# Kernel tuning notes

Hardware: AMD Instinct MI355X
Metric: run time of the kernel (lower is better)

Reference implementation:

```python
import jax, jax.numpy as jnp
import numpy as np

FS = 44100.0
# Time-constant bounds (seconds) hard-coded from RC component values in __init__
T_AF_MIN, T_AF_MAX = 820.0 * 4.7e-07 * 0.8, 270000.0 * 4.7e-07 * 1.2
T_AS_MIN, T_AS_MAX = 820.0 * 6.8e-06 * 0.8, 270000.0 * 6.8e-06 * 100.0
T_SF_MIN, T_SF_MAX = 91000.0 * 4.7e-07 * 0.8, 1200000.0 * 4.7e-07 * 1.2
T_SS_MIN, T_SS_MAX = 750000.0 * 6.8e-06 * 0.8, 750000.0 * 6.8e-06 * 100.0


def _logit(p):
    p = min(max(p, 1e-06), 1.0 - 1e-06)
    return float(np.log(p / (1.0 - p)))


def _u_from_seconds(val_s, tmin, tmax):
    return _logit((val_s - tmin) / (tmax - tmin))


def setup_inputs() -> dict:
    key = jax.random.key(0)
    B, T = 128, 131072
    # dB-domain peak envelope, roughly -60..+10 dB so the -24 dB threshold is exercised
    x = jax.random.normal(key, (B, T), dtype=jnp.float32) * 12.0 - 18.0
    return {
        'x_peak_dB': x,
        'comp_thresh': jnp.float32(-24.0),
        'ratio_logit': jnp.float32(np.log(4.0 - 1.0)),
        'fb_logit': jnp.float32(_logit(0.5)),
        'u_T_af': jnp.float32(_u_from_seconds(0.01, T_AF_MIN, T_AF_MAX)),
        'u_T_as': jnp.float32(_u_from_seconds(0.05, T_AS_MIN, T_AS_MAX)),
        'u_T_sf': jnp.float32(_u_from_seconds(0.03, T_SF_MIN, T_SF_MAX)),
        'u_T_ss': jnp.float32(_u_from_seconds(0.2, T_SS_MIN, T_SS_MAX)),
    }


def _secs(u, tmin, tmax):
    return tmin + (tmax - tmin) * jax.nn.sigmoid(u)


def _ssl_comp_gain(x, comp_thresh, ratio_logit, fb_logit, u_T_af, u_T_as, u_T_sf, u_T_ss):
    # Parameter reparameterization (matches module.forward)
    cr = jnp.maximum(jnp.exp(ratio_logit) + 1.0, 1.0 + 1e-04)
    fb = jnp.clip(jax.nn.sigmoid(fb_logit), 0.0, 1.0)
    a_af = jnp.exp(-1.0 / (FS * _secs(u_T_af, T_AF_MIN, T_AF_MAX)))
    a_as = jnp.exp(-1.0 / (FS * _secs(u_T_as, T_AS_MIN, T_AS_MAX)))
    a_sf = jnp.exp(-1.0 / (FS * _secs(u_T_sf, T_SF_MIN, T_SF_MAX)))
    a_ss = jnp.exp(-1.0 / (FS * _secs(u_T_ss, T_SS_MIN, T_SS_MAX)))
    slope = 1.0 - 1.0 / cr

    B = x.shape[0]
    z = jnp.zeros((B,), x.dtype)

    def step(carry, x_t):
        ef, es, y_prev = carry  # fast/slow envelope states (dB reduction, >=0), prev gain (dB)
        lvl = x_t + fb * y_prev              # feedback sidechain level (dB)
        tgt = jnp.maximum(lvl - comp_thresh, 0.0) * slope  # target gain reduction (dB)
        e = 0.5 * (ef + es)
        att = tgt > e                        # hard gate: attack vs shunt (release)
        af = jnp.where(att, a_af, a_sf)
        as_ = jnp.where(att, a_as, a_ss)
        ef = af * ef + (1.0 - af) * tgt
        es = as_ * es + (1.0 - as_) * tgt
        y = -0.5 * (ef + es)                 # gain in dB (<= 0)
        return (ef, es, y), y

    _, ys = jax.lax.scan(step, (z, z, z), x.T)  # scan over time, x.T: (T, B)
    return ys.T  # (B, T)


def reference(x_peak_dB, comp_thresh, ratio_logit, fb_logit, u_T_af, u_T_as, u_T_sf, u_T_ss):
    return _ssl_comp_gain(x_peak_dB.astype(jnp.float32), comp_thresh, ratio_logit,
                          fb_logit, u_T_af, u_T_as, u_T_sf, u_T_ss)
```

## Files before the change

kernel.cpp:

```cpp
#include <hip/hip_runtime.h>
#include <hip/hip_fp16.h>
#include <math.h>


constexpr int   T_LEN    = 131072;
constexpr int   NCM      = 64;
constexpr int   CM       = T_LEN / NCM;
constexpr int   SUB      = 16;
constexpr int   NC       = NCM * SUB;
constexpr int   CF       = T_LEN / NC;
constexpr int   K        = 16;
constexpr float STEP_ES  = 8.0f / 15.0f;
constexpr float INV_STEP = 15.0f / 8.0f;
constexpr int   DPF      = 8;
constexpr int   NV_ROW   = T_LEN >> 2;
constexpr int   NH_ROW   = T_LEN >> 3;
constexpr int   QROW     = T_LEN >> 2;
constexpr int   LINK     = NCM * K;

__device__ void compute_params(
        float* __restrict__ pw,
        const float* cth, const float* rl, const float* fbl,
        const float* uaf, const float* uas, const float* usf, const float* uss)
{
    const double FS = 44100.0;
    const double T_AF_MIN = 820.0 * 4.7e-07 * 0.8,   T_AF_MAX = 270000.0 * 4.7e-07 * 1.2;
    const double T_AS_MIN = 820.0 * 6.8e-06 * 0.8,   T_AS_MAX = 270000.0 * 6.8e-06 * 100.0;
    const double T_SF_MIN = 91000.0 * 4.7e-07 * 0.8, T_SF_MAX = 1200000.0 * 4.7e-07 * 1.2;
    const double T_SS_MIN = 750000.0 * 6.8e-06 * 0.8, T_SS_MAX = 750000.0 * 6.8e-06 * 100.0;

    double cr    = fmax(exp((double)rl[0]) + 1.0, 1.0 + 1e-4);
    double fb    = 1.0 / (1.0 + exp(-(double)fbl[0]));
    double slope = 1.0 - 1.0 / cr;

    double s_af = T_AF_MIN + (T_AF_MAX - T_AF_MIN) / (1.0 + exp(-(double)uaf[0]));
    double s_as = T_AS_MIN + (T_AS_MAX - T_AS_MIN) / (1.0 + exp(-(double)uas[0]));
    double s_sf = T_SF_MIN + (T_SF_MAX - T_SF_MIN) / (1.0 + exp(-(double)usf[0]));
    double s_ss = T_SS_MIN + (T_SS_MAX - T_SS_MIN) / (1.0 + exp(-(double)uss[0]));

    float a_af = (float)exp(-1.0 / (FS * s_af));
    float a_as = (float)exp(-1.0 / (FS * s_as));
    float a_sf = (float)exp(-1.0 / (FS * s_sf));
    float a_ss = (float)exp(-1.0 / (FS * s_ss));
    double q = 0.5 * slope * fb;

    pw[0]  = (float)(-0.5 * slope);
    pw[1]  = (float)(0.5 * slope * (double)cth[0]);
    pw[2]  = (float)(-q);
    pw[3]  = (float)(0.5 + q);
    pw[4]  = a_af;  pw[5] = a_as;  pw[6] = a_sf;  pw[7] = a_ss;
    float e_af = a_af * a_af, e_as = a_as * a_as, e_sf = a_sf * a_sf, e_ss = a_ss * a_ss;
    pw[8]  = e_af * e_af;  pw[9]  = e_as * e_as;
    pw[10] = e_sf * e_sf;  pw[11] = e_ss * e_ss;
    pw[12] = (float)(-0.125 * slope);
}

__device__ __forceinline__ void aff_compose(float4& A, float2& g,
                                            const float4 Bq, const float2 bg)
{
    float nx = Bq.x * A.x + Bq.y * A.z, ny = Bq.x * A.y + Bq.y * A.w;
    float nz = Bq.z * A.x + Bq.w * A.z, nw = Bq.z * A.y + Bq.w * A.w;
    float ngx = Bq.x * g.x + Bq.y * g.y + bg.x;
    float ngy = Bq.z * g.x + Bq.w * g.y + bg.y;
    A = make_float4(nx, ny, nz, nw); g = make_float2(ngx, ngy);
}

__global__ __launch_bounds__(256) void ssl_tr(
        const float* __restrict__ x, uint4* __restrict__ xth,
        float* __restrict__ xq, float* __restrict__ pw,
        const float* cth, const float* rl, const float* fbl,
        const float* uaf, const float* uas, const float* usf, const float* uss)
{
    if (blockIdx.x == 0 && threadIdx.x == 0)
        compute_params(pw, cth, rl, fbl, uaf, uas, usf, uss);

    __shared__ float4 lds4[64][33];
    const int b    = blockIdx.x >> 4;
    const int tile = blockIdx.x & 15;
    const int tid  = threadIdx.x;
    const int c0   = tile * 64;

    const float4* __restrict__ x4 = reinterpret_cast<const float4*>(x) + (size_t)b * NV_ROW;
    uint4* __restrict__ xtr       = xth + (size_t)b * NH_ROW;
    float* __restrict__ xqr       = xq + (size_t)b * QROW;

    #pragma unroll
    for (int it = 0; it < 8; ++it) {
        int idx = it * 256 + tid;
        int c = idx >> 5, s4 = idx & 31;
        float4 v = x4[(size_t)(c0 + c) * 32 + s4];
        lds4[c][s4] = v;
        xqr[(size_t)(c0 + c) * 32 + s4] = (v.x + v.y) + (v.z + v.w);
    }
    __syncthreads();
    #pragma unroll
    for (int it = 0; it < 4; ++it) {
        int idx = it * 256 + tid;
        int blk8 = idx >> 6, c = idx & 63;
        float4 a = lds4[c][2 * blk8];
        float4 d = lds4[c][2 * blk8 + 1];
        __half2 h0 = __floats2half2_rn(a.x, a.y);
        __half2 h1 = __floats2half2_rn(a.z, a.w);
        __half2 h2 = __floats2half2_rn(d.x, d.y);
        __half2 h3 = __floats2half2_rn(d.z, d.w);
        uint4 o;
        o.x = *reinterpret_cast<unsigned*>(&h0);
        o.y = *reinterpret_cast<unsigned*>(&h1);
        o.z = *reinterpret_cast<unsigned*>(&h2);
        o.w = *reinterpret_cast<unsigned*>(&h3);
        xtr[(size_t)blk8 * 1024 + c0 + c] = o;
    }
}

__global__ __launch_bounds__(256) void ssl_map_q(
        const float* __restrict__ xq, __half2* __restrict__ mp,
        const float* __restrict__ pw, int B)
{
    int tid = blockIdx.x * 256 + threadIdx.x;
    int k  = tid & (K - 1);
    int bc = tid >> 4;
    if (bc >= B * NCM) return;
    int c  = bc & (NCM - 1);
    int b  = bc >> 6;

    const float nhs_q = pw[12], hst = pw[1], nq = pw[2], r = pw[3];
    const float e_af = pw[8], e_as = pw[9], e_sf = pw[10], e_ss = pw[11];

    float v0s = -STEP_ES * (float)k;
    float EF = v0s, ES = v0s, Y = EF + ES;
    const float4* __restrict__ q4 =
        reinterpret_cast<const float4*>(xq) + (size_t)b * (QROW >> 2) + (size_t)c * (CM >> 4);

    float4 buf[DPF];
    #pragma unroll
    for (int i = 0; i < DPF; ++i) buf[i] = q4[i];

    #pragma unroll 1
    for (int s = 0; s < SUB; ++s) {
        #pragma unroll
        for (int i = 0; i < DPF; ++i) {
            float4 xv = buf[i];
            int nxt = s * DPF + DPF + i;
            if (nxt < (CM >> 4)) buf[i] = q4[nxt];
#define QSTEP(XS) { \
            float sx2 = fmaf(nhs_q, (XS), hst); \
            float u2  = fmaf(nq, Y, sx2); \
            float t2  = fminf(u2, 0.0f); \
            bool att  = sx2 < r * Y; \
            float af  = att ? e_af : e_sf; \
            float as2 = att ? e_as : e_ss; \
            EF = fmaf(af,  EF - t2, t2); \
            ES = fmaf(as2, ES - t2, t2); \
            Y  = EF + ES; }
            QSTEP(xv.x) QSTEP(xv.y) QSTEP(xv.z) QSTEP(xv.w)
#undef QSTEP
        }
        mp[((size_t)bc * SUB + s) * K + k] = __floats2half2_rn(EF, ES);
    }
}

__global__ __launch_bounds__(1024) void ssl_guess(
        const __half2* __restrict__ mp, float2* __restrict__ bnd,
        const float* __restrict__ pw, int B)
{
    __shared__ __half2 link_s[LINK];
    __shared__ float2 bnd_s[NC];
    const int b = blockIdx.x;
    const int t = threadIdx.x;

    {
        int c = t >> 4, k = t & 15;
        link_s[t] = mp[((size_t)(b * NCM + c) * SUB + (SUB - 1)) * K + k];
    }
    __syncthreads();

    if (t == 0) {
        float EF = 0.0f, ES = 0.0f;
        for (int c = 0; c < NCM; ++c) {
            bnd_s[SUB * c] = make_float2(EF, ES);
            float tt = -ES * INV_STEP;
            int idx = (int)tt;
            idx = idx < 0 ? 0 : (idx > K - 2 ? K - 2 : idx);
            float u = tt - (float)idx;
            float2 a0 = __half22float2(link_s[c * K + idx]);
            float2 a1 = __half22float2(link_s[c * K + idx + 1]);
            EF = a0.x + (a1.x - a0.x) * u;
            ES = a0.y + (a1.y - a0.y) * u;
        }
    }
    __syncthreads();
    {
        int c = t >> 4, j = t & 15;
        if (j > 0) {
            float ES = bnd_s[SUB * c].y;
            float tt = -ES * INV_STEP;
            int idx = (int)tt;
            idx = idx < 0 ? 0 : (idx > K - 2 ? K - 2 : idx);
            float u = tt - (float)idx;
            const __half2* m = mp + ((size_t)(b * NCM + c) * SUB + (j - 1)) * K;
            float2 a0 = __half22float2(m[idx]);
            float2 a1 = __half22float2(m[idx + 1]);
            bnd_s[t] = make_float2(a0.x + (a1.x - a0.x) * u,
                                   a0.y + (a1.y - a0.y) * u);
        }
    }
    __syncthreads();
    bnd[(size_t)b * NC + t] = bnd_s[t];
}

template<int MODE>
__global__ __launch_bounds__(256) void ssl_js(
        const uint4* __restrict__ xth,
        const float2* __restrict__ bnd0,
        const float4* __restrict__ Jin, const float2* __restrict__ gin,
        float4* __restrict__ Jout, float2* __restrict__ gout,
        float* __restrict__ out,
        const float* __restrict__ pw)
{
    const int blk = blockIdx.x;
    const int b = blk >> 2, j = blk & 3;
    const int tid = threadIdx.x;
    const int c = (j << 8) | tid;
    const int lane = tid & 63, w = tid >> 6;

    const float nhs = pw[0], hst = pw[1], nq = pw[2], r = pw[3];
    const float a_af = pw[4], a_as = pw[5], a_sf = pw[6], a_ss = pw[7];

    const uint4* __restrict__ baseh = xth + (size_t)b * NH_ROW;

    __shared__ float2 bnd_s[NC];
    __shared__ float4 wWJ[4];
    __shared__ float2 wWG[4];

    if (MODE >= 1) {
        const float4* Jr = Jin + (size_t)b * NC;
        const float2* gr = gin + (size_t)b * NC;
        float4 J0 = Jr[4 * tid + 0], J1 = Jr[4 * tid + 1],
               J2 = Jr[4 * tid + 2], J3 = Jr[4 * tid + 3];
        float2 g0 = gr[4 * tid + 0], g1 = gr[4 * tid + 1],
               g2 = gr[4 * tid + 2], g3 = gr[4 * tid + 3];

        float4 A = J0; float2 ag = g0;
        aff_compose(A, ag, J1, g1);
        aff_compose(A, ag, J2, g2);
        aff_compose(A, ag, J3, g3);

        float jFx = A.x, jFy = A.y, jSx = A.z, jSy = A.w, gx = ag.x, gy = ag.y;
        for (int d = 1; d < 64; d <<= 1) {
            float pa = __shfl_up(jFx, d), pb = __shfl_up(jFy, d);
            float pc = __shfl_up(jSx, d), pd = __shfl_up(jSy, d);
            float px = __shfl_up(gx, d),  py = __shfl_up(gy, d);
            if (lane >= d) {
                float na = jFx * pa + jFy * pc, nb = jFx * pb + jFy * pd;
                float nc = jSx * pa + jSy * pc, nd = jSx * pb + jSy * pd;
                gx = jFx * px + jFy * py + gx;
                gy = jSx * px + jSy * py + gy;
                jFx = na; jFy = nb; jSx = nc; jSy = nd;
            }
        }
        if (lane == 63) { wWJ[w] = make_float4(jFx, jFy, jSx, jSy); wWG[w] = make_float2(gx, gy); }
        __syncthreads();

        float2 v0 = make_float2(0.0f, 0.0f);
        for (int q = 0; q < w; ++q) {
            float4 Wq = wWJ[q]; float2 Wg = wWG[q];
            v0 = make_float2(Wq.x * v0.x + Wq.y * v0.y + Wg.x,
                             Wq.z * v0.x + Wq.w * v0.y + Wg.y);
        }
        float pa = __shfl_up(jFx, 1), pb = __shfl_up(jFy, 1);
        float pc = __shfl_up(jSx, 1), pd = __shfl_up(jSy, 1);
        float px = __shfl_up(gx, 1),  py = __shfl_up(gy, 1);
        float2 v;
        if (lane == 0) v = v0;
        else v = make_float2(pa * v0.x + pb * v0.y + px,
                             pc * v0.x + pd * v0.y + py);

        bnd_s[4 * tid + 0] = v;
        v = make_float2(J0.x * v.x + J0.y * v.y + g0.x, J0.z * v.x + J0.w * v.y + g0.y);
        bnd_s[4 * tid + 1] = v;
        v = make_float2(J1.x * v.x + J1.y * v.y + g1.x, J1.z * v.x + J1.w * v.y + g1.y);
        bnd_s[4 * tid + 2] = v;
        v = make_float2(J2.x * v.x + J2.y * v.y + g2.x, J2.z * v.x + J2.w * v.y + g2.y);
        bnd_s[4 * tid + 3] = v;
        __syncthreads();
    }

    float2 s0 = (MODE == 0) ? bnd0[(size_t)b * NC + c] : bnd_s[c];

    if (MODE <= 1) {
        float EF = s0.x, ES = s0.y, Y = EF + ES;
        float jFx = 1.0f, jFy = 0.0f, jSx = 0.0f, jSy = 1.0f;

        uint4 buf[DPF];
        #pragma unroll
        for (int i = 0; i < DPF; ++i) buf[i] = baseh[(size_t)i * 1024 + c];

        #pragma unroll 1
        for (int vb = 0; vb < 16; vb += DPF) {
            #pragma unroll
            for (int i = 0; i < DPF; ++i) {
                uint4 hv = buf[i];
                int nxt = vb + DPF + i;
                if (nxt < 16) buf[i] = baseh[(size_t)nxt * 1024 + c];
                const __half2* hp = reinterpret_cast<const __half2*>(&hv);
                float2 f0 = __half22float2(hp[0]);
                float2 f1 = __half22float2(hp[1]);
                float2 f2 = __half22float2(hp[2]);
                float2 f3 = __half22float2(hp[3]);
#define SSL_STEP_J(XV) { \
                float sx2 = fmaf(nhs, (XV), hst); \
                float u2  = fmaf(nq, Y, sx2); \
                float t2  = fminf(u2, 0.0f); \
                float mm  = (u2 < 0.0f) ? nq : 0.0f; \
                bool att  = sx2 < r * Y; \
                float af  = att ? a_af : a_sf; \
                float as2 = att ? a_as : a_ss; \
                float jtx = mm * (jFx + jSx); \
                float jty = mm * (jFy + jSy); \
                jFx = fmaf(af,  jFx - jtx, jtx); \
                jFy = fmaf(af,  jFy - jty, jty); \
                jSx = fmaf(as2, jSx - jtx, jtx); \
                jSy = fmaf(as2, jSy - jty, jty); \
                EF  = fmaf(af,  EF - t2, t2); \
                ES  = fmaf(as2, ES - t2, t2); \
                Y   = EF + ES; }
                SSL_STEP_J(f0.x) SSL_STEP_J(f0.y)
                SSL_STEP_J(f1.x) SSL_STEP_J(f1.y)
                SSL_STEP_J(f2.x) SSL_STEP_J(f2.y)
                SSL_STEP_J(f3.x) SSL_STEP_J(f3.y)
#undef SSL_STEP_J
            }
        }
        Jout[(size_t)b * NC + c] = make_float4(jFx, jFy, jSx, jSy);
        gout[(size_t)b * NC + c] = make_float2(EF - (jFx * s0.x + jFy * s0.y),
                                               ES - (jSx * s0.x + jSy * s0.y));
    } else {
        float EF = s0.x, ES = s0.y, Y = EF + ES;
        float4* __restrict__ yr = reinterpret_cast<float4*>(out) + (size_t)b * NV_ROW;

        uint4 buf[DPF];
        #pragma unroll
        for (int i = 0; i < DPF; ++i) buf[i] = baseh[(size_t)i * 1024 + c];

        #pragma unroll 1
        for (int vb = 0; vb < 16; vb += DPF) {
            #pragma unroll
            for (int i = 0; i < DPF; ++i) {
                uint4 hv = buf[i];
                int nxt = vb + DPF + i;
                if (nxt < 16) buf[i] = baseh[(size_t)nxt * 1024 + c];
                const __half2* hp = reinterpret_cast<const __half2*>(&hv);
                float2 f0 = __half22float2(hp[0]);
                float2 f1 = __half22float2(hp[1]);
                float2 f2 = __half22float2(hp[2]);
                float2 f3 = __half22float2(hp[3]);
                float4 yo0, yo1;
#define SSL_STEP(XV, YOUT) { \
                float sx2 = fmaf(nhs, (XV), hst); \
                float u2  = fmaf(nq, Y, sx2); \
                float t2  = fminf(u2, 0.0f); \
                bool att  = sx2 < r * Y; \
                float af  = att ? a_af : a_sf; \
                float as2 = att ? a_as : a_ss; \
                EF = fmaf(af,  EF - t2, t2); \
                ES = fmaf(as2, ES - t2, t2); \
                Y  = EF + ES; \
                (YOUT) = Y; }
                SSL_STEP(f0.x, yo0.x) SSL_STEP(f0.y, yo0.y)
                SSL_STEP(f1.x, yo0.z) SSL_STEP(f1.y, yo0.w)
                SSL_STEP(f2.x, yo1.x) SSL_STEP(f2.y, yo1.y)
                SSL_STEP(f3.x, yo1.z) SSL_STEP(f3.y, yo1.w)
#undef SSL_STEP
                yr[(size_t)c * 32 + 2 * (vb + i) + 0] = yo0;
                yr[(size_t)c * 32 + 2 * (vb + i) + 1] = yo1;
            }
        }
    }
}

extern "C" void kernel_launch(void* const* d_in, const int* in_sizes, int n_in,
                              void* d_out, int out_size, void* d_ws, size_t ws_size,
                              hipStream_t stream) {
    const float* x = (const float*)d_in[0];
    const int B = in_sizes[0] / T_LEN;
    const size_t NCt = (size_t)B * NC;

    const size_t MP_B = (size_t)B * NCM * SUB * K * sizeof(__half2);
    const size_t PW_O = MP_B;
    const size_t XQ_O = PW_O + 1024;
    const size_t XQ_B = (size_t)B * QROW * sizeof(float);
    const size_t XT_O = XQ_O + XQ_B;

    __half2* mp  = (__half2*)d_ws;
    float*   pw  = (float*)((char*)d_ws + PW_O);
    float*   xq  = (float*)((char*)d_ws + XQ_O);
    uint4*   xth = (uint4*)((char*)d_ws + XT_O);

    float2* bnd0 = (float2*)xq;
    float4* JvA  = (float4*)(bnd0 + NCt);
    float2* gvA  = (float2*)(JvA + NCt);
    float4* JvB  = (float4*)(gvA + NCt);
    float2* gvB  = (float2*)(JvB + NCt);

    ssl_tr<<<16 * B, 256, 0, stream>>>(
        x, xth, xq, pw,
        (const float*)d_in[1], (const float*)d_in[2], (const float*)d_in[3],
        (const float*)d_in[4], (const float*)d_in[5], (const float*)d_in[6],
        (const float*)d_in[7]);

    int map_blocks = (B * NCM * K + 255) / 256;
    ssl_map_q<<<map_blocks, 256, 0, stream>>>(xq, mp, pw, B);

    ssl_guess<<<B, 1024, 0, stream>>>(mp, bnd0, pw, B);

    const int NBLK = 4 * B;

    ssl_js<0><<<NBLK, 256, 0, stream>>>(xth, bnd0, nullptr, nullptr,
                                        JvA, gvA, nullptr, pw);
    ssl_js<1><<<NBLK, 256, 0, stream>>>(xth, nullptr, JvA, gvA,
                                        JvB, gvB, nullptr, pw);
    ssl_js<1><<<NBLK, 256, 0, stream>>>(xth, nullptr, JvB, gvB,
                                        JvA, gvA, nullptr, pw);
    ssl_js<2><<<NBLK, 256, 0, stream>>>(xth, nullptr, JvA, gvA,
                                        nullptr, nullptr, (float*)d_out, pw);
}
```

Baseline: 134.9 us.

## Store quad-summed input as fp16 and fold boundary-guess kernel into first sweep

The coarse quad-summed input buffer is now stored in half precision, halving its write and read traffic in the transpose and coarse-map kernels. The map kernel loads eight halves per vector and emits two map entries per outer iteration. The separate ssl_guess launch is removed; each ssl_js<0> block recomputes the coarse chain from the map and interpolates its own chunk start states. This saves one launch and a global round trip, but each of the four blocks per row now repeats the serial 64-step coarse scan, and fp16 rounding of the quad sums may affect accuracy of the initial guesses.

Measured after the change: 128.7 us. 1.05x faster.

```diff
diff --git a/kernel.cpp b/kernel.cpp
--- a/kernel.cpp
+++ b/kernel.cpp
@@ -67,7 +67,7 @@
 
 __global__ __launch_bounds__(256) void ssl_tr(
         const float* __restrict__ x, uint4* __restrict__ xth,
-        float* __restrict__ xq, float* __restrict__ pw,
+        __half* __restrict__ xq, float* __restrict__ pw,
         const float* cth, const float* rl, const float* fbl,
         const float* uaf, const float* uas, const float* usf, const float* uss)
 {
@@ -82,7 +82,7 @@
 
     const float4* __restrict__ x4 = reinterpret_cast<const float4*>(x) + (size_t)b * NV_ROW;
     uint4* __restrict__ xtr       = xth + (size_t)b * NH_ROW;
-    float* __restrict__ xqr       = xq + (size_t)b * QROW;
+    __half* __restrict__ xqr      = xq + (size_t)b * QROW;
 
     #pragma unroll
     for (int it = 0; it < 8; ++it) {
@@ -90,7 +90,7 @@
         int c = idx >> 5, s4 = idx & 31;
         float4 v = x4[(size_t)(c0 + c) * 32 + s4];
         lds4[c][s4] = v;
-        xqr[(size_t)(c0 + c) * 32 + s4] = (v.x + v.y) + (v.z + v.w);
+        xqr[(size_t)(c0 + c) * 32 + s4] = __float2half_rn((v.x + v.y) + (v.z + v.w));
     }
     __syncthreads();
     #pragma unroll
@@ -113,7 +113,7 @@
 }
 
 __global__ __launch_bounds__(256) void ssl_map_q(
-        const float* __restrict__ xq, __half2* __restrict__ mp,
+        const __half* __restrict__ xq, __half2* __restrict__ mp,
         const float* __restrict__ pw, int B)
 {
     int tid = blockIdx.x * 256 + threadIdx.x;
@@ -128,20 +128,25 @@
 
     float v0s = -STEP_ES * (float)k;
     float EF = v0s, ES = v0s, Y = EF + ES;
-    const float4* __restrict__ q4 =
-        reinterpret_cast<const float4*>(xq) + (size_t)b * (QROW >> 2) + (size_t)c * (CM >> 4);
-
-    float4 buf[DPF];
+    const uint4* __restrict__ q8 =
+        reinterpret_cast<const uint4*>(xq + (size_t)b * QROW + (size_t)c * (CM >> 2));
+
+    uint4 buf[DPF];
     #pragma unroll
-    for (int i = 0; i < DPF; ++i) buf[i] = q4[i];
+    for (int i = 0; i < DPF; ++i) buf[i] = q8[i];
 
     #pragma unroll 1
-    for (int s = 0; s < SUB; ++s) {
+    for (int g = 0; g < 8; ++g) {
         #pragma unroll
         for (int i = 0; i < DPF; ++i) {
-            float4 xv = buf[i];
-            int nxt = s * DPF + DPF + i;
-            if (nxt < (CM >> 4)) buf[i] = q4[nxt];
+            uint4 hv = buf[i];
+            int nxt = g * DPF + DPF + i;
+            if (nxt < 64) buf[i] = q8[nxt];
+            const __half2* hp = reinterpret_cast<const __half2*>(&hv);
+            float2 f0 = __half22float2(hp[0]);
+            float2 f1 = __half22float2(hp[1]);
+            float2 f2 = __half22float2(hp[2]);
+            float2 f3 = __half22float2(hp[3]);
 #define QSTEP(XS) { \
             float sx2 = fmaf(nhs_q, (XS), hst); \
             float u2  = fmaf(nq, Y, sx2); \
@@ -152,66 +157,20 @@
             EF = fmaf(af,  EF - t2, t2); \
             ES = fmaf(as2, ES - t2, t2); \
             Y  = EF + ES; }
-            QSTEP(xv.x) QSTEP(xv.y) QSTEP(xv.z) QSTEP(xv.w)
+            QSTEP(f0.x) QSTEP(f0.y) QSTEP(f1.x) QSTEP(f1.y)
+            QSTEP(f2.x) QSTEP(f2.y) QSTEP(f3.x) QSTEP(f3.y)
 #undef QSTEP
-        }
-        mp[((size_t)bc * SUB + s) * K + k] = __floats2half2_rn(EF, ES);
+            if (i == 3)
+                mp[((size_t)bc * SUB + 2 * g) * K + k] = __floats2half2_rn(EF, ES);
+        }
+        mp[((size_t)bc * SUB + 2 * g + 1) * K + k] = __floats2half2_rn(EF, ES);
     }
-}
-
-__global__ __launch_bounds__(1024) void ssl_guess(
-        const __half2* __restrict__ mp, float2* __restrict__ bnd,
-        const float* __restrict__ pw, int B)
-{
-    __shared__ __half2 link_s[LINK];
-    __shared__ float2 bnd_s[NC];
-    const int b = blockIdx.x;
-    const int t = threadIdx.x;
-
-    {
-        int c = t >> 4, k = t & 15;
-        link_s[t] = mp[((size_t)(b * NCM + c) * SUB + (SUB - 1)) * K + k];
-    }
-    __syncthreads();
-
-    if (t == 0) {
-        float EF = 0.0f, ES = 0.0f;
-        for (int c = 0; c < NCM; ++c) {
-            bnd_s[SUB * c] = make_float2(EF, ES);
-            float tt = -ES * INV_STEP;
-            int idx = (int)tt;
-            idx = idx < 0 ? 0 : (idx > K - 2 ? K - 2 : idx);
-            float u = tt - (float)idx;
-            float2 a0 = __half22float2(link_s[c * K + idx]);
-            float2 a1 = __half22float2(link_s[c * K + idx + 1]);
-            EF = a0.x + (a1.x - a0.x) * u;
-            ES = a0.y + (a1.y - a0.y) * u;
-        }
-    }
-    __syncthreads();
-    {
-        int c = t >> 4, j = t & 15;
-        if (j > 0) {
-            float ES = bnd_s[SUB * c].y;
-            float tt = -ES * INV_STEP;
-            int idx = (int)tt;
-            idx = idx < 0 ? 0 : (idx > K - 2 ? K - 2 : idx);
-            float u = tt - (float)idx;
-            const __half2* m = mp + ((size_t)(b * NCM + c) * SUB + (j - 1)) * K;
-            float2 a0 = __half22float2(m[idx]);
-            float2 a1 = __half22float2(m[idx + 1]);
-            bnd_s[t] = make_float2(a0.x + (a1.x - a0.x) * u,
-                                   a0.y + (a1.y - a0.y) * u);
-        }
-    }
-    __syncthreads();
-    bnd[(size_t)b * NC + t] = bnd_s[t];
 }
 
 template<int MODE>
 __global__ __launch_bounds__(256) void ssl_js(
         const uint4* __restrict__ xth,
-        const float2* __restrict__ bnd0,
+        const __half2* __restrict__ mp,
         const float4* __restrict__ Jin, const float2* __restrict__ gin,
         float4* __restrict__ Jout, float2* __restrict__ gout,
         float* __restrict__ out,
@@ -231,8 +190,49 @@
     __shared__ float2 bnd_s[NC];
     __shared__ float4 wWJ[4];
     __shared__ float2 wWG[4];
-
-    if (MODE >= 1) {
+    __shared__ __half2 link_s[LINK];
+    __shared__ float2 coarse_s[NCM];
+
+    float2 s0;
+
+    if (MODE == 0) {
+        #pragma unroll
+        for (int it = 0; it < LINK / 256; ++it) {
+            int i = it * 256 + tid;
+            int cc = i >> 4, kk = i & 15;
+            link_s[i] = mp[((size_t)(b * NCM + cc) * SUB + (SUB - 1)) * K + kk];
+        }
+        __syncthreads();
+        if (tid == 0) {
+            float EF = 0.0f, ES = 0.0f;
+            for (int cc = 0; cc < NCM; ++cc) {
+                coarse_s[cc] = make_float2(EF, ES);
+                float tt = -ES * INV_STEP;
+                int idx = (int)tt;
+                idx = idx < 0 ? 0 : (idx > K - 2 ? K - 2 : idx);
+                float u = tt - (float)idx;
+                float2 a0 = __half22float2(link_s[cc * K + idx]);
+                float2 a1 = __half22float2(link_s[cc * K + idx + 1]);
+                EF = a0.x + (a1.x - a0.x) * u;
+                ES = a0.y + (a1.y - a0.y) * u;
+            }
+        }
+        __syncthreads();
+        int cc = c >> 4, jj = c & 15;
+        float2 e = coarse_s[cc];
+        if (jj == 0) s0 = e;
+        else {
+            float tt = -e.y * INV_STEP;
+            int idx = (int)tt;
+            idx = idx < 0 ? 0 : (idx > K - 2 ? K - 2 : idx);
+            float u = tt - (float)idx;
+            const __half2* m = mp + ((size_t)(b * NCM + cc) * SUB + (jj - 1)) * K;
+            float2 a0 = __half22float2(m[idx]);
+            float2 a1 = __half22float2(m[idx + 1]);
+            s0 = make_float2(a0.x + (a1.x - a0.x) * u,
+                             a0.y + (a1.y - a0.y) * u);
+        }
+    } else {
         const float4* Jr = Jin + (size_t)b * NC;
         const float2* gr = gin + (size_t)b * NC;
         float4 J0 = Jr[4 * tid + 0], J1 = Jr[4 * tid + 1],
@@ -283,9 +283,8 @@
         v = make_float2(J2.x * v.x + J2.y * v.y + g2.x, J2.z * v.x + J2.w * v.y + g2.y);
         bnd_s[4 * tid + 3] = v;
         __syncthreads();
+        s0 = bnd_s[c];
     }
-
-    float2 s0 = (MODE == 0) ? bnd0[(size_t)b * NC + c] : bnd_s[c];
 
     if (MODE <= 1) {
         float EF = s0.x, ES = s0.y, Y = EF + ES;
@@ -388,16 +387,15 @@
     const size_t MP_B = (size_t)B * NCM * SUB * K * sizeof(__half2);
     const size_t PW_O = MP_B;
     const size_t XQ_O = PW_O + 1024;
-    const size_t XQ_B = (size_t)B * QROW * sizeof(float);
+    const size_t XQ_B = (size_t)B * QROW * sizeof(__half);
     const size_t XT_O = XQ_O + XQ_B;
 
     __half2* mp  = (__half2*)d_ws;
     float*   pw  = (float*)((char*)d_ws + PW_O);
-    float*   xq  = (float*)((char*)d_ws + XQ_O);
+    __half*  xq  = (__half*)((char*)d_ws + XQ_O);
     uint4*   xth = (uint4*)((char*)d_ws + XT_O);
 
-    float2* bnd0 = (float2*)xq;
-    float4* JvA  = (float4*)(bnd0 + NCt);
+    float4* JvA  = (float4*)xq;
     float2* gvA  = (float2*)(JvA + NCt);
     float4* JvB  = (float4*)(gvA + NCt);
     float2* gvB  = (float2*)(JvB + NCt);
@@ -411,11 +409,9 @@
     int map_blocks = (B * NCM * K + 255) / 256;
     ssl_map_q<<<map_blocks, 256, 0, stream>>>(xq, mp, pw, B);
 
-    ssl_guess<<<B, 1024, 0, stream>>>(mp, bnd0, pw, B);
-
     const int NBLK = 4 * B;
 
-    ssl_js<0><<<NBLK, 256, 0, stream>>>(xth, bnd0, nullptr, nullptr,
+    ssl_js<0><<<NBLK, 256, 0, stream>>>(xth, mp, nullptr, nullptr,
                                         JvA, gvA, nullptr, pw);
     ssl_js<1><<<NBLK, 256, 0, stream>>>(xth, nullptr, JvA, gvA,
                                         JvB, gvB, nullptr, pw);
```
